# Performance work log

Hardware: AMD Instinct MI355X
Metric: run time of the kernel (lower is better)

The kernel has to match this reference:

```python
import jax
import jax.numpy as jnp
from jax import lax
import numpy as np

DIM = 64
HIDDEN = int(DIM * 2.66)      # 170
C2 = HIDDEN * 2               # 340
PATCH = 8


def setup_inputs() -> dict:
    key = jax.random.key(0)
    k1, k2, k3, k4, k5 = jax.random.split(key, 5)
    B, H, W = 4, 256, 256
    x = jax.random.normal(k1, (B, DIM, H, W), dtype=jnp.float32)
    # project_in: 1x1 conv, stored as [out, in]
    w_in = jax.random.normal(k2, (C2, DIM), dtype=jnp.float32) * (1.0 / np.sqrt(DIM))
    # depthwise 3x3 conv weight [C2, 1, 3, 3]
    w_dw = jax.random.normal(k3, (C2, 1, 3, 3), dtype=jnp.float32) * (1.0 / 3.0)
    # learned rFFT filter, init ones in torch; perturb for a nontrivial test
    fft_w = 1.0 + 0.1 * jax.random.normal(k4, (C2, 1, 1, PATCH, PATCH // 2 + 1), dtype=jnp.float32)
    # project_out: 1x1 conv [out, in]
    w_out = jax.random.normal(k5, (DIM, HIDDEN), dtype=jnp.float32) * (1.0 / np.sqrt(HIDDEN))
    return {"x": x, "w_in": w_in, "w_dw": w_dw, "fft_w": fft_w, "w_out": w_out}


def reference(x, w_in, w_dw, fft_w, w_out):
    p = PATCH
    # project_in (1x1 conv)
    x = jnp.einsum('bchw,oc->bohw', x, w_in)
    B, C, H, W = x.shape
    # patchify: b c (h p1) (w p2) -> b c h w p1 p2
    xp = x.reshape(B, C, H // p, p, W // p, p).transpose(0, 1, 2, 4, 3, 5)
    # per-patch rFFT2, elementwise learned filter, inverse
    xf = jnp.fft.rfft2(xp)                       # [B,C,h,w,8,5] complex
    xf = xf * fft_w                              # fft_w broadcasts [C,1,1,8,5]
    xp = jnp.fft.irfft2(xf, s=(p, p))
    # unpatchify
    x = xp.transpose(0, 1, 2, 4, 3, 5).reshape(B, C, H, W)
    # depthwise 3x3 conv, padding 1
    x = lax.conv_general_dilated(
        x, w_dw, window_strides=(1, 1), padding=((1, 1), (1, 1)),
        dimension_numbers=('NCHW', 'OIHW', 'NCHW'), feature_group_count=C)
    # GELU gate
    x1, x2 = jnp.split(x, 2, axis=1)
    x = jax.nn.gelu(x1, approximate=False) * x2
    # project_out (1x1 conv)
    return jnp.einsum('bchw,oc->bohw', x, w_out)
```

## Files before the change

kernel.cpp:

```cpp
#include <hip/hip_runtime.h>
#include <hip/hip_bf16.h>

#define C2 340
#define HID 170
#define NB 4
#define HGT 256
#define WID 256
#define HW (HGT*WID)
#define BAND 128

typedef unsigned short u16;
typedef unsigned int u32;
typedef float f32x4 __attribute__((ext_vector_type(4)));
typedef short s16x8 __attribute__((ext_vector_type(8)));

__device__ __forceinline__ float bf2f(u16 u) {
  union { u32 i; float f; } v; v.i = ((u32)u) << 16; return v.f;
}
__device__ __forceinline__ u16 f2bf(float f) {
  union { float f; u32 i; } v; v.f = f;
  u32 x = v.i;
  return (u16)((x + 0x7fffu + ((x >> 16) & 1u)) >> 16);
}

__device__ const float COSTAB[8] = {1.f, 0.70710678118654752f, 0.f, -0.70710678118654752f,
                                    -1.f, -0.70710678118654752f, 0.f, 0.70710678118654752f};

__global__ __launch_bounds__(256) void k_prep(const float* __restrict__ w_in,
                                              const float* __restrict__ w_out,
                                              const float* __restrict__ fw,
                                              u16* __restrict__ wf,
                                              u16* __restrict__ wof,
                                              u16* __restrict__ mf) {
  __shared__ float kern[64];
  const int blk = blockIdx.x;
  if (blk < C2) {
    const int c = blk;
    if (threadIdx.x < 64) {
      const int a = threadIdx.x >> 3, bb = threadIdx.x & 7;
      float acc = 0.f;
      for (int u = 0; u < 8; ++u)
        for (int v = 0; v < 8; ++v) {
          const float wv = (v <= 4) ? fw[c*40 + u*5 + v]
                                    : fw[c*40 + ((8-u)&7)*5 + (8-v)];
          acc += wv * COSTAB[(u*a + v*bb) & 7];
        }
      kern[threadIdx.x] = acc * (1.f/64.f);
    }
    __syncthreads();
    #pragma unroll
    for (int q = 0; q < 16; ++q) {
      const int e = q * 256 + threadIdx.x;
      const int r = e & 7;
      const int l = (e >> 3) & 63;
      const int sb = e >> 9;
      const int s = sb & 1, nblk = sb >> 1;
      const int k = s*32 + ((l >> 4) << 3) + r;
      const int a = k >> 3, bcol = k & 7;
      const int n = nblk*16 + (l & 15);
      const int i = n >> 3, j = n & 7;
      mf[(size_t)c * 4096 + e] = f2bf(kern[(((i - a) & 7) << 3) + ((j - bcol) & 7)]);
    }
  } else if (blk == C2) {
    for (int e = threadIdx.x; e < 22*2*64*8; e += 256) {
      const int r = e & 7;
      const int l = (e >> 3) & 63;
      const int ts = e >> 9;
      const int s = ts & 1, t = ts >> 1;
      const int m = t*16 + (l & 15);
      const int k = s*32 + ((l >> 4) << 3) + r;
      wf[e] = (m < C2) ? f2bf(w_in[m*64 + k]) : (u16)0;
    }
  } else {
    for (int e = threadIdx.x; e < 4*6*64*8; e += 256) {
      const int r = e & 7;
      const int l = (e >> 3) & 63;
      const int mk = e >> 9;
      const int kc = mk % 6, mt = mk / 6;
      const int m = mt*16 + (l & 15);
      const int k = kc*32 + ((l >> 4) << 3) + r;
      wof[e] = (k < HID) ? f2bf(w_out[m*HID + k]) : (u16)0;
    }
  }
}

__global__ __launch_bounds__(256) void k_projin2(const float* __restrict__ x,
                                                 const u16* __restrict__ wf,
                                                 u16* __restrict__ mid) {
  __shared__ __align__(16) u16 st[16][264];
  const int b = blockIdx.x >> 8;
  const int pix_blk = (blockIdx.x & 255) << 8;
  const int w = threadIdx.x >> 6;
  const int lane = threadIdx.x & 63;
  const int lm = lane & 15, lh = lane >> 4;
  const int pix0 = pix_blk + w*64;

  s16x8 Bf[4][2];
  {
    const float* xp = x + (size_t)b * 64 * HW + pix0;
    #pragma unroll
    for (int g = 0; g < 4; ++g)
      #pragma unroll
      for (int s = 0; s < 2; ++s) {
        s16x8 t;
        #pragma unroll
        for (int r = 0; r < 8; ++r) {
          const int ch = s*32 + lh*8 + r;
          t[r] = (short)f2bf(xp[(size_t)ch * HW + g*16 + lm]);
        }
        Bf[g][s] = t;
      }
  }
  u16* mp = mid + (size_t)b * C2 * HW + pix_blk;
  const int ch_rd = threadIdx.x >> 4;
  const int seg = threadIdx.x & 15;
  for (int t = 0; t < 22; ++t) {
    const s16x8 A0 = *(const s16x8*)(wf + ((t*2 + 0)*64 + lane)*8);
    const s16x8 A1 = *(const s16x8*)(wf + ((t*2 + 1)*64 + lane)*8);
    f32x4 ac[4];
    #pragma unroll
    for (int g = 0; g < 4; ++g) {
      ac[g] = (f32x4){0.f,0.f,0.f,0.f};
      ac[g] = __builtin_amdgcn_mfma_f32_16x16x32_bf16(A0, Bf[g][0], ac[g], 0,0,0);
      ac[g] = __builtin_amdgcn_mfma_f32_16x16x32_bf16(A1, Bf[g][1], ac[g], 0,0,0);
    }
    __syncthreads();
    #pragma unroll
    for (int g = 0; g < 4; ++g)
      #pragma unroll
      for (int r = 0; r < 4; ++r)
        st[lh*4 + r][w*64 + g*16 + lm] = f2bf(ac[g][r]);
    __syncthreads();
    const int ch = t*16 + ch_rd;
    if (ch < C2) {
      u16* dst = mp + (size_t)ch * HW + seg*16;
      *(uint4*)dst       = *(const uint4*)&st[ch_rd][seg*16];
      *(uint4*)(dst + 8) = *(const uint4*)&st[ch_rd][seg*16 + 8];
    }
  }
}

__global__ __launch_bounds__(256) void k_pconv2(u16* __restrict__ mid,
                                                const u16* __restrict__ mf) {
  __shared__ __align__(16) u16 st[16][264];
  const int gid = blockIdx.x;
  const int half = gid & 1;
  const int bc = gid >> 1;
  const int c = bc % C2;
  const int lane = threadIdx.x & 63;
  const int w = threadIdx.x >> 6;
  u16* chan = mid + (size_t)bc * HW;

  s16x8 Bf[4][2];
  const u16* mfc = mf + (size_t)c * 4096;
  #pragma unroll
  for (int nb = 0; nb < 4; ++nb)
    #pragma unroll
    for (int s = 0; s < 2; ++s)
      Bf[nb][s] = *(const s16x8*)(mfc + ((nb*2 + s)*64 + lane)*8);

  const int lm = lane & 15, lh = lane >> 4;
  const int rr = threadIdx.x >> 4;
  const int seg = threadIdx.x & 15;
  for (int it = 0; it < 8; ++it) {
    const int pg = half*512 + (it*4 + w)*16;
    const int py = pg >> 5, px0 = pg & 31;
    const u16* aptr = chan + (size_t)(py*8 + lh)*WID + (px0 + lm)*8;
    const s16x8 A0 = *(const s16x8*)(aptr);
    const s16x8 A1 = *(const s16x8*)(aptr + 4*WID);
    f32x4 ac0 = {0.f,0.f,0.f,0.f}, ac1 = {0.f,0.f,0.f,0.f};
    f32x4 ac2 = {0.f,0.f,0.f,0.f}, ac3 = {0.f,0.f,0.f,0.f};
    ac0 = __builtin_amdgcn_mfma_f32_16x16x32_bf16(A0, Bf[0][0], ac0, 0,0,0);
    ac0 = __builtin_amdgcn_mfma_f32_16x16x32_bf16(A1, Bf[0][1], ac0, 0,0,0);
    ac1 = __builtin_amdgcn_mfma_f32_16x16x32_bf16(A0, Bf[1][0], ac1, 0,0,0);
    ac1 = __builtin_amdgcn_mfma_f32_16x16x32_bf16(A1, Bf[1][1], ac1, 0,0,0);
    ac2 = __builtin_amdgcn_mfma_f32_16x16x32_bf16(A0, Bf[2][0], ac2, 0,0,0);
    ac2 = __builtin_amdgcn_mfma_f32_16x16x32_bf16(A1, Bf[2][1], ac2, 0,0,0);
    ac3 = __builtin_amdgcn_mfma_f32_16x16x32_bf16(A0, Bf[3][0], ac3, 0,0,0);
    ac3 = __builtin_amdgcn_mfma_f32_16x16x32_bf16(A1, Bf[3][1], ac3, 0,0,0);
    __syncthreads();
    const int colbase = ((w & 1)*16 + lh*4)*8 + (lm & 7);
    const int rowbase = (w >> 1)*8 + (lm >> 3);
    #pragma unroll
    for (int r = 0; r < 4; ++r) {
      st[rowbase + 0][colbase + r*8] = f2bf(ac0[r]);
      st[rowbase + 2][colbase + r*8] = f2bf(ac1[r]);
      st[rowbase + 4][colbase + r*8] = f2bf(ac2[r]);
      st[rowbase + 6][colbase + r*8] = f2bf(ac3[r]);
    }
    __syncthreads();
    const int row0 = half*128 + it*16;
    u16* dst = chan + (size_t)(row0 + rr)*WID + seg*16;
    *(uint4*)dst       = *(const uint4*)&st[rr][seg*16];
    *(uint4*)(dst + 8) = *(const uint4*)&st[rr][seg*16 + 8];
  }
}

__global__ __launch_bounds__(256) void k_gate(const u16* __restrict__ mid,
                                              const float* __restrict__ w_dw,
                                              u16* __restrict__ gbuf, int hb) {
  __shared__ __align__(16) u16 sh[2][10][272];
  const int s  = blockIdx.x & 15;
  const int bc = blockIdx.x >> 4;
  const int c  = bc % HID, b = bc / HID;
  const int h0 = hb + s * 8;

  for (int i = threadIdx.x; i < 2*10*34; i += 256)
    ((uint4*)sh)[i] = make_uint4(0,0,0,0);
  __syncthreads();
  for (int i = threadIdx.x; i < 640; i += 256) {
    const int sg = i & 31;
    const int r = (i >> 5) % 10;
    const int ch2 = i / 320;
    const int h = h0 + r - 1;
    if (h >= 0 && h < HGT)
      *(uint4*)&sh[ch2][r][8 + sg*8] =
        *(const uint4*)(mid + ((size_t)(b*C2 + c + ch2*HID)) * HW + (size_t)h * WID + sg*8);
  }
  __syncthreads();

  const int rg = threadIdx.x >> 5;
  const int cg = threadIdx.x & 31;
  const int px0 = cg * 8;
  const float* wd1 = w_dw + c * 9;
  const float* wd2 = w_dw + (c + HID) * 9;

  float ax[8], ay[8];
  #pragma unroll
  for (int p = 0; p < 8; ++p) { ax[p] = 0.f; ay[p] = 0.f; }
  #pragma unroll
  for (int wr = 0; wr < 3; ++wr) {
    const u16* r1 = &sh[0][rg + wr][px0];
    const u16* r2 = &sh[1][rg + wr][px0];
    const s16x8 L1 = *(const s16x8*)r1, M1 = *(const s16x8*)(r1 + 8), R1 = *(const s16x8*)(r1 + 16);
    const s16x8 L2 = *(const s16x8*)r2, M2 = *(const s16x8*)(r2 + 8), R2 = *(const s16x8*)(r2 + 16);
    float cx[10], cy[10];
    cx[0] = bf2f((u16)L1[7]);  cy[0] = bf2f((u16)L2[7]);
    #pragma unroll
    for (int p = 0; p < 8; ++p) { cx[p+1] = bf2f((u16)M1[p]); cy[p+1] = bf2f((u16)M2[p]); }
    cx[9] = bf2f((u16)R1[0]);  cy[9] = bf2f((u16)R2[0]);
    const float w1a = wd1[wr*3+0], w1b = wd1[wr*3+1], w1c = wd1[wr*3+2];
    const float w2a = wd2[wr*3+0], w2b = wd2[wr*3+1], w2c = wd2[wr*3+2];
    #pragma unroll
    for (int p = 0; p < 8; ++p) {
      ax[p] += w1a*cx[p] + w1b*cx[p+1] + w1c*cx[p+2];
      ay[p] += w2a*cy[p] + w2b*cy[p+1] + w2c*cy[p+2];
    }
  }
  u32 pk[4];
  #pragma unroll
  for (int p2 = 0; p2 < 4; ++p2) {
    float g0 = 0.5f * ax[2*p2]   * (1.f + erff(ax[2*p2]   * 0.70710678118654752f)) * ay[2*p2];
    float g1 = 0.5f * ax[2*p2+1] * (1.f + erff(ax[2*p2+1] * 0.70710678118654752f)) * ay[2*p2+1];
    pk[p2] = (u32)f2bf(g0) | ((u32)f2bf(g1) << 16);
  }
  u16* gp = gbuf + (((size_t)(b*HID + c)) * BAND + (size_t)(s*8 + rg)) * WID + px0;
  *(uint4*)gp = make_uint4(pk[0], pk[1], pk[2], pk[3]);
}

__global__ __launch_bounds__(256) void k_projout2(const u16* __restrict__ gbuf,
                                                  const u16* __restrict__ wof,
                                                  float* __restrict__ out, int hb) {
  const int b = blockIdx.x >> 7;
  const int p0 = (blockIdx.x & 127) << 8;
  const int w = threadIdx.x >> 6;
  const int lane = threadIdx.x & 63;
  const int lm = lane & 15, lh = lane >> 4;
  const size_t BW = (size_t)BAND * WID;
  const u16* gb = gbuf + (size_t)b * HID * BW + p0 + w*64 + lm;

  f32x4 acc[4][4];
  #pragma unroll
  for (int mt = 0; mt < 4; ++mt)
    #pragma unroll
    for (int ng = 0; ng < 4; ++ng)
      acc[mt][ng] = (f32x4){0.f,0.f,0.f,0.f};

  #pragma unroll
  for (int kc = 0; kc < 6; ++kc) {
    s16x8 A[4];
    #pragma unroll
    for (int mt = 0; mt < 4; ++mt)
      A[mt] = *(const s16x8*)(wof + ((mt*6 + kc)*64 + lane)*8);
    #pragma unroll
    for (int ng = 0; ng < 4; ++ng) {
      s16x8 Bf;
      #pragma unroll
      for (int r = 0; r < 8; ++r) {
        int c = kc*32 + lh*8 + r;
        if (kc == 5) c = min(c, HID - 1);
        Bf[r] = (short)gb[(size_t)c * BW + ng*16];
      }
      #pragma unroll
      for (int mt = 0; mt < 4; ++mt)
        acc[mt][ng] = __builtin_amdgcn_mfma_f32_16x16x32_bf16(A[mt], Bf, acc[mt][ng], 0,0,0);
    }
  }
  float* ob = out + (size_t)b * 64 * HW + (size_t)hb * WID + p0 + w*64 + lm;
  #pragma unroll
  for (int mt = 0; mt < 4; ++mt)
    #pragma unroll
    for (int ng = 0; ng < 4; ++ng)
      #pragma unroll
      for (int r = 0; r < 4; ++r)
        ob[(size_t)(mt*16 + lh*4 + r) * HW + ng*16] = acc[mt][ng][r];
}

extern "C" void kernel_launch(void* const* d_in, const int* in_sizes, int n_in,
                              void* d_out, int out_size, void* d_ws, size_t ws_size,
                              hipStream_t stream) {
  const float* x     = (const float*)d_in[0];
  const float* w_in  = (const float*)d_in[1];
  const float* w_dw  = (const float*)d_in[2];
  const float* fw    = (const float*)d_in[3];
  const float* w_out = (const float*)d_in[4];
  float* out = (float*)d_out;

  char* ws = (char*)d_ws;
  u16* mid    = (u16*)ws;
  u16* gbuf   = (u16*)(ws + 178257920);
  u16* wof    = (u16*)(ws + 178257920 + 44564480);
  u16* mfrag  = (u16*)(ws + 178257920 + 44564480 + 43520);
  u16* wfrag  = (u16*)(ws + 178257920 + 44564480 + 43520 + 2785280);

  k_prep<<<C2 + 2, 256, 0, stream>>>(w_in, w_out, fw, wfrag, wof, mfrag);
  k_projin2<<<NB*256, 256, 0, stream>>>(x, wfrag, mid);
  k_pconv2<<<NB*C2*2, 256, 0, stream>>>(mid, mfrag);
  for (int sb = 0; sb < 2; ++sb) {
    const int hb = sb * BAND;
    k_gate<<<NB*HID*16, 256, 0, stream>>>(mid, w_dw, gbuf, hb);
    k_projout2<<<NB*BAND, 256, 0, stream>>>(gbuf, wof, out, hb);
  }
}
```

Before: 255.4 us.

## Fuse patch FFT filter matmul into depthwise-conv GELU gate kernel

Removes the separate in-place per-patch filter pass over the mid buffer and instead applies the patch-filter MFMA inside the gate kernel. Each block handles one (batch, channel pair) and walks down the 128-row band in steps of 16 rows, keeping a rolling halo row in shared memory and recomputing the neighbouring patch rows that the 3x3 stencil needs. This avoids one full read and write of the 340-channel intermediate. In exchange it recomputes some halo patches, launches far fewer blocks (NB*HID of 512 threads), and adds more barriers per iteration, which may lower occupancy and parallelism.

```diff
diff --git a/kernel.cpp b/kernel.cpp
--- a/kernel.cpp
+++ b/kernel.cpp
@@ -140,122 +140,138 @@
   }
 }
 
-__global__ __launch_bounds__(256) void k_pconv2(u16* __restrict__ mid,
-                                                const u16* __restrict__ mf) {
-  __shared__ __align__(16) u16 st[16][264];
-  const int gid = blockIdx.x;
-  const int half = gid & 1;
-  const int bc = gid >> 1;
-  const int c = bc % C2;
+__global__ __launch_bounds__(512) void k_pcgate(const u16* __restrict__ mid,
+                                                const u16* __restrict__ mf,
+                                                const float* __restrict__ w_dw,
+                                                u16* __restrict__ gbuf, int hb) {
+  __shared__ __align__(16) u16 st[2][18][272];
+  const int c = blockIdx.x % HID;
+  const int b = blockIdx.x / HID;
+  const int P0 = hb >> 3;
+
+  const int w = threadIdx.x >> 6;
   const int lane = threadIdx.x & 63;
-  const int w = threadIdx.x >> 6;
-  u16* chan = mid + (size_t)bc * HW;
-
-  s16x8 Bf[4][2];
-  const u16* mfc = mf + (size_t)c * 4096;
+  const int lm = lane & 15, lh = lane >> 4;
+  const int ch2 = w >> 2;
+  const int wl = w & 3;
+  const int prow_sub = wl >> 1;
+  const int phalf = wl & 1;
+  const int ch = c + ch2*HID;
+  const int colbase = (phalf*16 + lh*4)*8 + (lm & 7) + 8;
+
+  for (int i = threadIdx.x; i < 2*18*34; i += 512)
+    ((uint4*)st)[i] = make_uint4(0,0,0,0);
+
+  s16x8 Bc[4][2];
+  const u16* mfc = mf + (size_t)ch * 4096;
   #pragma unroll
   for (int nb = 0; nb < 4; ++nb)
     #pragma unroll
-    for (int s = 0; s < 2; ++s)
-      Bf[nb][s] = *(const s16x8*)(mfc + ((nb*2 + s)*64 + lane)*8);
-
-  const int lm = lane & 15, lh = lane >> 4;
-  const int rr = threadIdx.x >> 4;
-  const int seg = threadIdx.x & 15;
-  for (int it = 0; it < 8; ++it) {
-    const int pg = half*512 + (it*4 + w)*16;
-    const int py = pg >> 5, px0 = pg & 31;
-    const u16* aptr = chan + (size_t)(py*8 + lh)*WID + (px0 + lm)*8;
-    const s16x8 A0 = *(const s16x8*)(aptr);
-    const s16x8 A1 = *(const s16x8*)(aptr + 4*WID);
-    f32x4 ac0 = {0.f,0.f,0.f,0.f}, ac1 = {0.f,0.f,0.f,0.f};
-    f32x4 ac2 = {0.f,0.f,0.f,0.f}, ac3 = {0.f,0.f,0.f,0.f};
-    ac0 = __builtin_amdgcn_mfma_f32_16x16x32_bf16(A0, Bf[0][0], ac0, 0,0,0);
-    ac0 = __builtin_amdgcn_mfma_f32_16x16x32_bf16(A1, Bf[0][1], ac0, 0,0,0);
-    ac1 = __builtin_amdgcn_mfma_f32_16x16x32_bf16(A0, Bf[1][0], ac1, 0,0,0);
-    ac1 = __builtin_amdgcn_mfma_f32_16x16x32_bf16(A1, Bf[1][1], ac1, 0,0,0);
-    ac2 = __builtin_amdgcn_mfma_f32_16x16x32_bf16(A0, Bf[2][0], ac2, 0,0,0);
-    ac2 = __builtin_amdgcn_mfma_f32_16x16x32_bf16(A1, Bf[2][1], ac2, 0,0,0);
-    ac3 = __builtin_amdgcn_mfma_f32_16x16x32_bf16(A0, Bf[3][0], ac3, 0,0,0);
-    ac3 = __builtin_amdgcn_mfma_f32_16x16x32_bf16(A1, Bf[3][1], ac3, 0,0,0);
-    __syncthreads();
-    const int colbase = ((w & 1)*16 + lh*4)*8 + (lm & 7);
-    const int rowbase = (w >> 1)*8 + (lm >> 3);
-    #pragma unroll
-    for (int r = 0; r < 4; ++r) {
-      st[rowbase + 0][colbase + r*8] = f2bf(ac0[r]);
-      st[rowbase + 2][colbase + r*8] = f2bf(ac1[r]);
-      st[rowbase + 4][colbase + r*8] = f2bf(ac2[r]);
-      st[rowbase + 6][colbase + r*8] = f2bf(ac3[r]);
-    }
-    __syncthreads();
-    const int row0 = half*128 + it*16;
-    u16* dst = chan + (size_t)(row0 + rr)*WID + seg*16;
-    *(uint4*)dst       = *(const uint4*)&st[rr][seg*16];
-    *(uint4*)(dst + 8) = *(const uint4*)&st[rr][seg*16 + 8];
-  }
-}
-
-__global__ __launch_bounds__(256) void k_gate(const u16* __restrict__ mid,
-                                              const float* __restrict__ w_dw,
-                                              u16* __restrict__ gbuf, int hb) {
-  __shared__ __align__(16) u16 sh[2][10][272];
-  const int s  = blockIdx.x & 15;
-  const int bc = blockIdx.x >> 4;
-  const int c  = bc % HID, b = bc / HID;
-  const int h0 = hb + s * 8;
-
-  for (int i = threadIdx.x; i < 2*10*34; i += 256)
-    ((uint4*)sh)[i] = make_uint4(0,0,0,0);
-  __syncthreads();
-  for (int i = threadIdx.x; i < 640; i += 256) {
-    const int sg = i & 31;
-    const int r = (i >> 5) % 10;
-    const int ch2 = i / 320;
-    const int h = h0 + r - 1;
-    if (h >= 0 && h < HGT)
-      *(uint4*)&sh[ch2][r][8 + sg*8] =
-        *(const uint4*)(mid + ((size_t)(b*C2 + c + ch2*HID)) * HW + (size_t)h * WID + sg*8);
-  }
-  __syncthreads();
-
-  const int rg = threadIdx.x >> 5;
-  const int cg = threadIdx.x & 31;
-  const int px0 = cg * 8;
+    for (int ks = 0; ks < 2; ++ks)
+      Bc[nb][ks] = *(const s16x8*)(mfc + ((nb*2 + ks)*64 + lane)*8);
+  const u16* chan = mid + (size_t)(b*C2 + ch) * HW;
   const float* wd1 = w_dw + c * 9;
   const float* wd2 = w_dw + (c + HID) * 9;
-
-  float ax[8], ay[8];
-  #pragma unroll
-  for (int p = 0; p < 8; ++p) { ax[p] = 0.f; ay[p] = 0.f; }
-  #pragma unroll
-  for (int wr = 0; wr < 3; ++wr) {
-    const u16* r1 = &sh[0][rg + wr][px0];
-    const u16* r2 = &sh[1][rg + wr][px0];
-    const s16x8 L1 = *(const s16x8*)r1, M1 = *(const s16x8*)(r1 + 8), R1 = *(const s16x8*)(r1 + 16);
-    const s16x8 L2 = *(const s16x8*)r2, M2 = *(const s16x8*)(r2 + 8), R2 = *(const s16x8*)(r2 + 16);
-    float cx[10], cy[10];
-    cx[0] = bf2f((u16)L1[7]);  cy[0] = bf2f((u16)L2[7]);
-    #pragma unroll
-    for (int p = 0; p < 8; ++p) { cx[p+1] = bf2f((u16)M1[p]); cy[p+1] = bf2f((u16)M2[p]); }
-    cx[9] = bf2f((u16)R1[0]);  cy[9] = bf2f((u16)R2[0]);
-    const float w1a = wd1[wr*3+0], w1b = wd1[wr*3+1], w1c = wd1[wr*3+2];
-    const float w2a = wd2[wr*3+0], w2b = wd2[wr*3+1], w2c = wd2[wr*3+2];
-    #pragma unroll
-    for (int p = 0; p < 8; ++p) {
-      ax[p] += w1a*cx[p] + w1b*cx[p+1] + w1c*cx[p+2];
-      ay[p] += w2a*cy[p] + w2b*cy[p+1] + w2c*cy[p+2];
-    }
-  }
-  u32 pk[4];
-  #pragma unroll
-  for (int p2 = 0; p2 < 4; ++p2) {
-    float g0 = 0.5f * ax[2*p2]   * (1.f + erff(ax[2*p2]   * 0.70710678118654752f)) * ay[2*p2];
-    float g1 = 0.5f * ax[2*p2+1] * (1.f + erff(ax[2*p2+1] * 0.70710678118654752f)) * ay[2*p2+1];
-    pk[p2] = (u32)f2bf(g0) | ((u32)f2bf(g1) << 16);
-  }
-  u16* gp = gbuf + (((size_t)(b*HID + c)) * BAND + (size_t)(s*8 + rg)) * WID + px0;
-  *(uint4*)gp = make_uint4(pk[0], pk[1], pk[2], pk[3]);
+  __syncthreads();
+
+  for (int it = 0; it < 8; ++it) {
+    const int py2 = P0 + it*2 + 2;
+    if (it == 0) {
+      for (int i = threadIdx.x; i < 2*34; i += 512)
+        ((uint4*)&st[i/34][0][0])[i%34] = make_uint4(0,0,0,0);
+    } else {
+      for (int i = threadIdx.x; i < 2*34; i += 512)
+        ((uint4*)&st[i/34][0][0])[i%34] = ((const uint4*)&st[i/34][16][0])[i%34];
+    }
+    if (py2 >= 32) {
+      for (int i = threadIdx.x; i < 2*34; i += 512)
+        ((uint4*)&st[i/34][17][0])[i%34] = make_uint4(0,0,0,0);
+    }
+    __syncthreads();
+    {
+      const int py = P0 + it*2 + prow_sub;
+      const u16* aptr = chan + (size_t)(py*8 + lh)*WID + (phalf*16 + lm)*8;
+      const s16x8 A0 = *(const s16x8*)(aptr);
+      const s16x8 A1 = *(const s16x8*)(aptr + 4*WID);
+      const int rowb = 1 + prow_sub*8 + (lm >> 3);
+      #pragma unroll
+      for (int nb = 0; nb < 4; ++nb) {
+        f32x4 acc = {0.f,0.f,0.f,0.f};
+        acc = __builtin_amdgcn_mfma_f32_16x16x32_bf16(A0, Bc[nb][0], acc, 0,0,0);
+        acc = __builtin_amdgcn_mfma_f32_16x16x32_bf16(A1, Bc[nb][1], acc, 0,0,0);
+        #pragma unroll
+        for (int r = 0; r < 4; ++r)
+          st[ch2][rowb + nb*2][colbase + r*8] = f2bf(acc[r]);
+      }
+    }
+    if (wl < 2) {
+      if (py2 < 32) {
+        const u16* ap = chan + (size_t)(py2*8 + lh)*WID + (phalf*16 + lm)*8;
+        const s16x8 A0 = *(const s16x8*)(ap);
+        const s16x8 A1 = *(const s16x8*)(ap + 4*WID);
+        f32x4 acc = {0.f,0.f,0.f,0.f};
+        acc = __builtin_amdgcn_mfma_f32_16x16x32_bf16(A0, Bc[0][0], acc, 0,0,0);
+        acc = __builtin_amdgcn_mfma_f32_16x16x32_bf16(A1, Bc[0][1], acc, 0,0,0);
+        if ((lm >> 3) == 0) {
+          #pragma unroll
+          for (int r = 0; r < 4; ++r)
+            st[ch2][17][colbase + r*8] = f2bf(acc[r]);
+        }
+      }
+    } else if (it == 0) {
+      const int pym = P0 - 1;
+      if (pym >= 0) {
+        const u16* ap = chan + (size_t)(pym*8 + lh)*WID + (phalf*16 + lm)*8;
+        const s16x8 A0 = *(const s16x8*)(ap);
+        const s16x8 A1 = *(const s16x8*)(ap + 4*WID);
+        f32x4 acc = {0.f,0.f,0.f,0.f};
+        acc = __builtin_amdgcn_mfma_f32_16x16x32_bf16(A0, Bc[3][0], acc, 0,0,0);
+        acc = __builtin_amdgcn_mfma_f32_16x16x32_bf16(A1, Bc[3][1], acc, 0,0,0);
+        if ((lm >> 3) == 1) {
+          #pragma unroll
+          for (int r = 0; r < 4; ++r)
+            st[ch2][0][colbase + r*8] = f2bf(acc[r]);
+        }
+      }
+    }
+    __syncthreads();
+    {
+      const int rg = threadIdx.x >> 5;
+      const int px0 = (threadIdx.x & 31) * 8;
+      float ax[8], ay[8];
+      #pragma unroll
+      for (int p = 0; p < 8; ++p) { ax[p] = 0.f; ay[p] = 0.f; }
+      #pragma unroll
+      for (int wr = 0; wr < 3; ++wr) {
+        const u16* r1 = &st[0][rg + wr][px0];
+        const u16* r2 = &st[1][rg + wr][px0];
+        const s16x8 L1 = *(const s16x8*)r1, M1 = *(const s16x8*)(r1 + 8), R1 = *(const s16x8*)(r1 + 16);
+        const s16x8 L2 = *(const s16x8*)r2, M2 = *(const s16x8*)(r2 + 8), R2 = *(const s16x8*)(r2 + 16);
+        float cx[10], cy[10];
+        cx[0] = bf2f((u16)L1[7]);  cy[0] = bf2f((u16)L2[7]);
+        #pragma unroll
+        for (int p = 0; p < 8; ++p) { cx[p+1] = bf2f((u16)M1[p]); cy[p+1] = bf2f((u16)M2[p]); }
+        cx[9] = bf2f((u16)R1[0]);  cy[9] = bf2f((u16)R2[0]);
+        const float w1a = wd1[wr*3+0], w1b = wd1[wr*3+1], w1c = wd1[wr*3+2];
+        const float w2a = wd2[wr*3+0], w2b = wd2[wr*3+1], w2c = wd2[wr*3+2];
+        #pragma unroll
+        for (int p = 0; p < 8; ++p) {
+          ax[p] += w1a*cx[p] + w1b*cx[p+1] + w1c*cx[p+2];
+          ay[p] += w2a*cy[p] + w2b*cy[p+1] + w2c*cy[p+2];
+        }
+      }
+      u32 pk[4];
+      #pragma unroll
+      for (int p2 = 0; p2 < 4; ++p2) {
+        float g0 = 0.5f * ax[2*p2]   * (1.f + erff(ax[2*p2]   * 0.70710678118654752f)) * ay[2*p2];
+        float g1 = 0.5f * ax[2*p2+1] * (1.f + erff(ax[2*p2+1] * 0.70710678118654752f)) * ay[2*p2+1];
+        pk[p2] = (u32)f2bf(g0) | ((u32)f2bf(g1) << 16);
+      }
+      u16* gp = gbuf + (((size_t)(b*HID + c)) * BAND + (size_t)(it*16 + rg)) * WID + px0;
+      *(uint4*)gp = make_uint4(pk[0], pk[1], pk[2], pk[3]);
+    }
+    __syncthreads();
+  }
 }
 
 __global__ __launch_bounds__(256) void k_projout2(const u16* __restrict__ gbuf,
@@ -325,10 +341,9 @@
 
   k_prep<<<C2 + 2, 256, 0, stream>>>(w_in, w_out, fw, wfrag, wof, mfrag);
   k_projin2<<<NB*256, 256, 0, stream>>>(x, wfrag, mid);
-  k_pconv2<<<NB*C2*2, 256, 0, stream>>>(mid, mfrag);
   for (int sb = 0; sb < 2; ++sb) {
     const int hb = sb * BAND;
-    k_gate<<<NB*HID*16, 256, 0, stream>>>(mid, w_dw, gbuf, hb);
+    k_pcgate<<<NB*HID, 512, 0, stream>>>(mid, mfrag, w_dw, gbuf, hb);
     k_projout2<<<NB*BAND, 256, 0, stream>>>(gbuf, wof, out, hb);
   }
 }
```

Result: faster. 249.9 us (-2.1%).
